# Performance work log

Measured on AMD Instinct MI355X. Metric: run time of the kernel, lower is better.

Reference implementation:

```python
import jax, jax.numpy as jnp
import numpy as np
from jax import lax

DIM = 128
N_CODEBOOKS = 8
CODEBOOK_SIZE = 2048
BATCH = 16
TOKENS = 2048


def setup_inputs() -> dict:
    key = jax.random.key(0)
    k1, k2 = jax.random.split(key)
    x = jax.random.normal(k1, (BATCH, DIM, TOKENS), dtype=jnp.float32)
    # matches nn.Parameter(torch.randn(K, D) / D**0.5) per stage, stacked
    codebooks = jax.random.normal(k2, (N_CODEBOOKS, CODEBOOK_SIZE, DIM),
                                  dtype=jnp.float32) / jnp.sqrt(jnp.float32(DIM))
    return {"x": x, "codebooks": codebooks}


def reference(x, codebooks):
    """Residual VQ forward.

    x: (B, D, T), codebooks: (n_cb, K, D)
    Returns (total_quantized (B,D,T), codes (B,n_cb,T) int32, commitment_loss scalar)
    """
    xt = jnp.transpose(x, (0, 2, 1))  # (B, T, D)

    def step(carry, cb):
        residual, total = carry  # (B,T,D) each; cb: (K,D)
        # squared euclidean distances: ||r||^2 - 2 r.c + ||c||^2 -> (B,T,K)
        dist = (jnp.sum(residual * residual, axis=-1, keepdims=True)
                - 2.0 * jnp.einsum('btd,kd->btk', residual, cb)
                + jnp.sum(cb * cb, axis=-1))
        idx = jnp.argmin(dist, axis=-1)          # (B, T)
        quantized = cb[idx]                       # gather -> (B, T, D)
        # straight-through combine
        q_st = residual + lax.stop_gradient(quantized - residual)
        total = total + q_st
        residual = residual - lax.stop_gradient(quantized)
        # F.mse_loss(residual.detach(), zeros) == mean(residual**2), detached
        loss = jnp.mean(lax.stop_gradient(residual) ** 2)
        return (residual, total), (idx.astype(jnp.int32), loss)

    init = (xt, jnp.zeros_like(xt))
    (_, total), (codes, losses) = lax.scan(step, init, codebooks)
    total_quantized = jnp.transpose(total, (0, 2, 1))   # (B, D, T)
    codes = jnp.transpose(codes, (1, 0, 2))             # (B, n_cb, T)
    commitment_loss = jnp.sum(losses)
    return total_quantized, codes, commitment_loss
```

## Files before the change

### kernel.cpp

```cpp
#include <hip/hip_runtime.h>

#define DIM 128
#define NCB 8
#define KSZ 2048
#define BATCH 16
#define TOK 2048
#define NTOK (BATCH * TOK)
#define NELEM (BATCH * DIM * TOK)
#define T_TILE 64
#define NTHR 256
#define CHUNK 64
#define NCHUNK (KSZ / CHUNK)

typedef float f32x4 __attribute__((ext_vector_type(4)));
typedef short s16x8 __attribute__((ext_vector_type(8)));

__device__ __forceinline__ unsigned short f2bf(float f) {
    unsigned u = __float_as_uint(f);
    u = (u + 0x7FFFu + ((u >> 16) & 1u)) >> 16;
    return (unsigned short)u;
}
__device__ __forceinline__ float bf2f(unsigned short h) {
    return __uint_as_float(((unsigned)h) << 16);
}

__global__ void rvq_prep_hi(const float* __restrict__ cbs,
                            unsigned short* __restrict__ ch) {
    int i = blockIdx.x * 256 + threadIdx.x;
    ch[i] = f2bf(cbs[i]);
}

__global__ void rvq_cnorm(const float* __restrict__ cbs,
                          float* __restrict__ cnorm,
                          float* __restrict__ loss_acc) {
    if (blockIdx.x == 0 && threadIdx.x == 0) *loss_acc = 0.0f;
    int k = blockIdx.x * 256 + threadIdx.x;
    const float4* row = (const float4*)(cbs + (size_t)k * DIM);
    float s = 0.0f;
#pragma unroll
    for (int i = 0; i < DIM / 4; ++i) {
        float4 v = row[i];
        s += v.x * v.x + v.y * v.y + v.z * v.z + v.w * v.w;
    }
    cnorm[k] = s;
}

__global__ __launch_bounds__(NTHR, 2) void rvq_fused(
        const float* __restrict__ x,
        const float* __restrict__ cbs,
        const unsigned short* __restrict__ ch,
        const float* __restrict__ cng,
        float* __restrict__ out,
        float* __restrict__ codes,
        float* __restrict__ loss_acc) {
    __shared__ float res_lds[T_TILE][DIM + 2];
    __shared__ unsigned short Bbuf[2][8192];
    __shared__ float mv1[T_TILE * 16];
    __shared__ float mv2[T_TILE * 16];
    __shared__ unsigned short mi1[T_TILE * 16];
    __shared__ unsigned short mi2[T_TILE * 16];

    const int tid   = threadIdx.x;
    const int lane  = tid & 63;
    const int wv    = __builtin_amdgcn_readfirstlane(tid >> 6);
    const int col16 = lane & 15;
    const int quad  = lane >> 4;

    const int token0 = blockIdx.x * T_TILE;
    const int b      = token0 >> 11;
    const int t_in_b = token0 & (TOK - 1);

    {
        const float* xb = x + (size_t)b * DIM * TOK + t_in_b;
#pragma unroll
        for (int it = 0; it < 8; ++it) {
            int idx = it * NTHR + tid;
            int d  = idx >> 4;
            int t4 = (idx & 15) * 4;
            float4 v = *(const float4*)(xb + (size_t)d * TOK + t4);
            res_lds[t4 + 0][d] = v.x;
            res_lds[t4 + 1][d] = v.y;
            res_lds[t4 + 2][d] = v.z;
            res_lds[t4 + 3][d] = v.w;
        }
    }
    __syncthreads();

    float my_loss = 0.0f;

#define STAGE_PREFETCH(cc)                                                     \
    {                                                                          \
        const unsigned short* _p = ch_s +                                      \
            ((size_t)((cc) * CHUNK + wv * 16 + col16)) * DIM + quad * 8;       \
        stg0 = *(const s16x8*)(_p + 0);                                        \
        stg1 = *(const s16x8*)(_p + 32);                                       \
        stg2 = *(const s16x8*)(_p + 64);                                       \
        stg3 = *(const s16x8*)(_p + 96);                                       \
    }

#define STAGE_WRITE(buf)                                                       \
    {                                                                          \
        *(s16x8*)&Bbuf[buf][(wv * 4 + 0) * 512 + lane * 8] = stg0;             \
        *(s16x8*)&Bbuf[buf][(wv * 4 + 1) * 512 + lane * 8] = stg1;             \
        *(s16x8*)&Bbuf[buf][(wv * 4 + 2) * 512 + lane * 8] = stg2;             \
        *(s16x8*)&Bbuf[buf][(wv * 4 + 3) * 512 + lane * 8] = stg3;             \
    }

#define COMPUTE(accv, buf)                                                     \
    {                                                                          \
        _Pragma("unroll")                                                      \
        for (int nt = 0; nt < 4; ++nt) accv[nt] = (f32x4){0.f, 0.f, 0.f, 0.f}; \
        _Pragma("unroll")                                                      \
        for (int dc = 0; dc < 4; ++dc) {                                       \
            s16x8 bh0 = *(const s16x8*)&Bbuf[buf][(0 + dc) * 512 + lane * 8];  \
            s16x8 bh1 = *(const s16x8*)&Bbuf[buf][(4 + dc) * 512 + lane * 8];  \
            s16x8 bh2 = *(const s16x8*)&Bbuf[buf][(8 + dc) * 512 + lane * 8];  \
            s16x8 bh3 = *(const s16x8*)&Bbuf[buf][(12 + dc) * 512 + lane * 8]; \
            accv[0] = __builtin_amdgcn_mfma_f32_16x16x32_bf16(ah[dc], bh0, accv[0], 0, 0, 0); \
            accv[1] = __builtin_amdgcn_mfma_f32_16x16x32_bf16(ah[dc], bh1, accv[1], 0, 0, 0); \
            accv[2] = __builtin_amdgcn_mfma_f32_16x16x32_bf16(ah[dc], bh2, accv[2], 0, 0, 0); \
            accv[3] = __builtin_amdgcn_mfma_f32_16x16x32_bf16(ah[dc], bh3, accv[3], 0, 0, 0); \
            accv[0] = __builtin_amdgcn_mfma_f32_16x16x32_bf16(al[dc], bh0, accv[0], 0, 0, 0); \
            accv[1] = __builtin_amdgcn_mfma_f32_16x16x32_bf16(al[dc], bh1, accv[1], 0, 0, 0); \
            accv[2] = __builtin_amdgcn_mfma_f32_16x16x32_bf16(al[dc], bh2, accv[2], 0, 0, 0); \
            accv[3] = __builtin_amdgcn_mfma_f32_16x16x32_bf16(al[dc], bh3, accv[3], 0, 0, 0); \
        }                                                                      \
    }

#define FOLD(accv, cc)                                                         \
    {                                                                          \
        int _ib0 = (cc) * CHUNK + col16;                                       \
        float _cn0 = cn_s[_ib0], _cn1 = cn_s[_ib0 + 16];                       \
        float _cn2 = cn_s[_ib0 + 32], _cn3 = cn_s[_ib0 + 48];                  \
        _Pragma("unroll")                                                      \
        for (int r = 0; r < 4; ++r) {                                          \
            float p0 = fmaf(-2.0f, accv[0][r], _cn0);                          \
            float p1 = fmaf(-2.0f, accv[1][r], _cn1);                          \
            float p2 = fmaf(-2.0f, accv[2][r], _cn2);                          \
            float p3 = fmaf(-2.0f, accv[3][r], _cn3);                          \
            bool c01 = p1 < p0;                                                \
            float m01 = c01 ? p1 : p0; int j01 = c01 ? _ib0 + 16 : _ib0;       \
            bool c23 = p3 < p2;                                                \
            float m23 = c23 ? p3 : p2; int j23 = c23 ? _ib0 + 48 : _ib0 + 32;  \
            bool cf = m23 < m01;                                               \
            float m = cf ? m23 : m01; int jm = cf ? j23 : j01;                 \
            bool b1 = m < v1[r];                                               \
            bool b2 = m < v2[r];                                               \
            v2[r] = b1 ? v1[r] : (b2 ? m : v2[r]);                             \
            i2[r] = b1 ? i1[r] : (b2 ? jm : i2[r]);                            \
            v1[r] = b1 ? m : v1[r];                                            \
            i1[r] = b1 ? jm : i1[r];                                           \
        }                                                                      \
    }

#pragma unroll 1
    for (int s = 0; s < NCB; ++s) {
        const unsigned short* __restrict__ ch_s = ch  + (size_t)s * KSZ * DIM;
        const float* __restrict__ cb_s = cbs + (size_t)s * KSZ * DIM;
        const float* __restrict__ cn_s = cng + (size_t)s * KSZ;

        s16x8 ah[4], al[4];
#pragma unroll
        for (int dc = 0; dc < 4; ++dc) {
            int t  = wv * 16 + col16;
            int d0 = dc * 32 + quad * 8;
            float4 u = *(const float4*)&res_lds[t][d0];
            float4 w = *(const float4*)&res_lds[t][d0 + 4];
            float e[8] = {u.x, u.y, u.z, u.w, w.x, w.y, w.z, w.w};
            s16x8 hv, lv;
#pragma unroll
            for (int j = 0; j < 8; ++j) {
                unsigned short h = f2bf(e[j]);
                hv[j] = (short)h;
                lv[j] = (short)f2bf(e[j] - bf2f(h));
            }
            ah[dc] = hv;
            al[dc] = lv;
        }

        float v1[4], v2[4]; int i1[4], i2[4];
#pragma unroll
        for (int r = 0; r < 4; ++r) {
            v1[r] = 3.4e38f; v2[r] = 3.4e38f; i1[r] = 0; i2[r] = 0;
        }

        s16x8 stg0, stg1, stg2, stg3;
        f32x4 accA[4], accB[4];

        STAGE_PREFETCH(0); STAGE_WRITE(0); __syncthreads();
        STAGE_PREFETCH(1);
        COMPUTE(accA, 0);
        STAGE_WRITE(1); __syncthreads();
#pragma unroll 1
        for (int c = 1; c < 31; c += 2) {
            STAGE_PREFETCH(c + 1);
            COMPUTE(accB, 1);
            FOLD(accA, c - 1);
            STAGE_WRITE(0);
            __syncthreads();
            STAGE_PREFETCH(c + 2);
            COMPUTE(accA, 0);
            FOLD(accB, c);
            STAGE_WRITE(1);
            __syncthreads();
        }
        COMPUTE(accB, 1);
        FOLD(accA, 30);
        FOLD(accB, 31);

#pragma unroll
        for (int r = 0; r < 4; ++r) {
            int t = wv * 16 + quad * 4 + r;
            mv1[t * 16 + col16] = v1[r];
            mi1[t * 16 + col16] = (unsigned short)i1[r];
            mv2[t * 16 + col16] = v2[r];
            mi2[t * 16 + col16] = (unsigned short)i2[r];
        }
        __syncthreads();

        const int t  = tid >> 2;
        const int cs = tid & 3;
        float bv[4] = {3.4e38f, 3.4e38f, 3.4e38f, 3.4e38f};
        int   bi[4] = {0x7FFFFFFF, 0x7FFFFFFF, 0x7FFFFFFF, 0x7FFFFFFF};
        {
            const float4 cv1 = *(const float4*)&mv1[tid * 4];
            const float4 cv2 = *(const float4*)&mv2[tid * 4];
            const unsigned short* ci1 = &mi1[tid * 4];
            const unsigned short* ci2 = &mi2[tid * 4];
            float vv[8] = {cv1.x, cv1.y, cv1.z, cv1.w,
                           cv2.x, cv2.y, cv2.z, cv2.w};
            int   ii[8] = {ci1[0], ci1[1], ci1[2], ci1[3],
                           ci2[0], ci2[1], ci2[2], ci2[3]};
#pragma unroll
            for (int c = 0; c < 8; ++c) {
                float v = vv[c]; int i = ii[c];
#pragma unroll
                for (int j = 0; j < 4; ++j) {
                    if (v < bv[j] || (v == bv[j] && i < bi[j])) {
                        float tv = bv[j]; bv[j] = v; v = tv;
                        int   ti = bi[j]; bi[j] = i; i = ti;
                    }
                }
            }
#pragma unroll
            for (int mk = 1; mk <= 2; mk <<= 1) {
                float ov[4]; int oi[4];
#pragma unroll
                for (int j = 0; j < 4; ++j) {
                    ov[j] = __shfl_xor(bv[j], mk, 64);
                    oi[j] = __shfl_xor(bi[j], mk, 64);
                }
#pragma unroll
                for (int c = 0; c < 4; ++c) {
                    float v = ov[c]; int i = oi[c];
#pragma unroll
                    for (int j = 0; j < 4; ++j) {
                        if (v < bv[j] || (v == bv[j] && i < bi[j])) {
                            float tv = bv[j]; bv[j] = v; v = tv;
                            int   ti = bi[j]; bi[j] = i; i = ti;
                        }
                    }
                }
            }
        }
        const int cand = (cs == 0) ? bi[0]
                       : (cs == 1) ? bi[1]
                       : (cs == 2) ? bi[2] : bi[3];

        {
            const float* crow = cb_s + (size_t)cand * DIM;
            float n0 = 0, n1 = 0, n2 = 0, n3 = 0;
            float a0 = 0, a1 = 0, a2 = 0, a3 = 0;
#pragma unroll 8
            for (int d4 = 0; d4 < DIM / 4; ++d4) {
                float4 r4 = *(const float4*)&res_lds[t][d4 * 4];
                float4 q4 = *(const float4*)&crow[d4 * 4];
                n0 = fmaf(r4.x, r4.x, n0); n1 = fmaf(r4.y, r4.y, n1);
                n2 = fmaf(r4.z, r4.z, n2); n3 = fmaf(r4.w, r4.w, n3);
                a0 = fmaf(r4.x, q4.x, a0); a1 = fmaf(r4.y, q4.y, a1);
                a2 = fmaf(r4.z, q4.z, a2); a3 = fmaf(r4.w, q4.w, a3);
            }
            float rn  = (n0 + n1) + (n2 + n3);
            float dot = (a0 + a1) + (a2 + a3);
            float dist = fmaf(-2.0f, dot, rn) + cn_s[cand];
            int best = cand;
#pragma unroll
            for (int mk = 1; mk <= 2; mk <<= 1) {
                float od = __shfl_xor(dist, mk, 64);
                int   oi = __shfl_xor(best, mk, 64);
                if (od < dist || (od == dist && oi < best)) {
                    dist = od; best = oi;
                }
            }
            if (cs == 0)
                codes[(size_t)b * (NCB * TOK) + (size_t)s * TOK + t_in_b + t] =
                    (float)best;
            const float* qrow = cb_s + (size_t)best * DIM;
            float lp = 0.0f;
#pragma unroll
            for (int d4 = 0; d4 < 8; ++d4) {
                int d = cs * 32 + d4 * 4;
                float4 r4 = *(const float4*)&res_lds[t][d];
                float4 q4 = *(const float4*)&qrow[d];
                float4 nr;
                nr.x = r4.x - q4.x; nr.y = r4.y - q4.y;
                nr.z = r4.z - q4.z; nr.w = r4.w - q4.w;
                *(float4*)&res_lds[t][d] = nr;
                lp += nr.x * nr.x + nr.y * nr.y + nr.z * nr.z + nr.w * nr.w;
            }
            my_loss += lp;
        }
        __syncthreads();
    }

    {
        const float* xb = x + (size_t)b * DIM * TOK + t_in_b;
        float* ob = out + (size_t)b * DIM * TOK + t_in_b;
#pragma unroll
        for (int it = 0; it < 8; ++it) {
            int idx = it * NTHR + tid;
            int d  = idx >> 4;
            int t4 = (idx & 15) * 4;
            float4 v = *(const float4*)(xb + (size_t)d * TOK + t4);
            float4 o;
            o.x = v.x - res_lds[t4 + 0][d];
            o.y = v.y - res_lds[t4 + 1][d];
            o.z = v.z - res_lds[t4 + 2][d];
            o.w = v.w - res_lds[t4 + 3][d];
            *(float4*)(ob + (size_t)d * TOK + t4) = o;
        }
    }

#pragma unroll
    for (int off = 32; off > 0; off >>= 1)
        my_loss += __shfl_down(my_loss, off, 64);
    if (lane == 0) atomicAdd(loss_acc, my_loss);
}

__global__ void rvq_loss_fin(const float* __restrict__ loss_acc,
                             float* __restrict__ loss_out) {
    *loss_out = *loss_acc * (1.0f / (float)NELEM);
}

extern "C" void kernel_launch(void* const* d_in, const int* in_sizes, int n_in,
                              void* d_out, int out_size, void* d_ws, size_t ws_size,
                              hipStream_t stream) {
    const float* x   = (const float*)d_in[0];
    const float* cbs = (const float*)d_in[1];

    float* out      = (float*)d_out;
    float* codes    = out + NELEM;
    float* loss_out = out + NELEM + (size_t)BATCH * NCB * TOK;

    float* wsf      = (float*)d_ws;
    float* loss_acc = wsf;
    unsigned short* ch = (unsigned short*)(wsf + 256);
    float* cng = (float*)(ch + (size_t)NCB * KSZ * DIM);

    hipLaunchKernelGGL(rvq_prep_hi, dim3((NCB * KSZ * DIM) / 256), dim3(256),
                       0, stream, cbs, ch);
    hipLaunchKernelGGL(rvq_cnorm, dim3((NCB * KSZ) / 256), dim3(256), 0, stream,
                       cbs, cng, loss_acc);
    hipLaunchKernelGGL(rvq_fused, dim3(NTOK / T_TILE), dim3(NTHR), 0, stream,
                       x, cbs, ch, cng, out, codes, loss_acc);
    hipLaunchKernelGGL(rvq_loss_fin, dim3(1), dim3(1), 0, stream,
                       loss_acc, loss_out);
}
```

Measured before the change: 511.5 us.

## Split codebook search across wave pairs with 512-thread blocks

Doubles the block to 512 threads. Each pair of waves shares a 16-token row group, and each wave of the pair scans one half of the codebook in 32-code chunks. The per-token top-2 merge and exact rerank are widened to 8 lanes per token, with a shared-memory handoff of the top-4 candidates. The intent is more waves in flight to hide latency. The cost is dropping the old two-accumulator software pipeline that overlapped the MFMA compute with the fold, and adding two barriers per chunk.

Result: slower. 571.8 us (+11.8%).

```diff
diff --git a/kernel.cpp b/kernel.cpp
--- a/kernel.cpp
+++ b/kernel.cpp
@@ -8,9 +8,9 @@
 #define NTOK (BATCH * TOK)
 #define NELEM (BATCH * DIM * TOK)
 #define T_TILE 64
-#define NTHR 256
-#define CHUNK 64
-#define NCHUNK (KSZ / CHUNK)
+#define NTHR 512
+#define CHUNK 32
+#define HCHUNKS 32
 
 typedef float f32x4 __attribute__((ext_vector_type(4)));
 typedef short s16x8 __attribute__((ext_vector_type(8)));
@@ -45,7 +45,7 @@
     cnorm[k] = s;
 }
 
-__global__ __launch_bounds__(NTHR, 2) void rvq_fused(
+__global__ __launch_bounds__(NTHR, 4) void rvq_fused(
         const float* __restrict__ x,
         const float* __restrict__ cbs,
         const unsigned short* __restrict__ ch,
@@ -54,17 +54,20 @@
         float* __restrict__ codes,
         float* __restrict__ loss_acc) {
     __shared__ float res_lds[T_TILE][DIM + 2];
-    __shared__ unsigned short Bbuf[2][8192];
-    __shared__ float mv1[T_TILE * 16];
-    __shared__ float mv2[T_TILE * 16];
-    __shared__ unsigned short mi1[T_TILE * 16];
-    __shared__ unsigned short mi2[T_TILE * 16];
+    __shared__ unsigned short Bbuf[2][4096];
+    __shared__ float mv1[T_TILE * 32];
+    __shared__ float mv2[T_TILE * 32];
+    __shared__ unsigned short mi1[T_TILE * 32];
+    __shared__ unsigned short mi2[T_TILE * 32];
+    __shared__ unsigned short best4s[T_TILE][4];
 
     const int tid   = threadIdx.x;
     const int lane  = tid & 63;
     const int wv    = __builtin_amdgcn_readfirstlane(tid >> 6);
     const int col16 = lane & 15;
     const int quad  = lane >> 4;
+    const int h2    = wv & 1;
+    const int wg    = wv >> 1;
 
     const int token0 = blockIdx.x * T_TILE;
     const int b      = token0 >> 11;
@@ -73,7 +76,7 @@
     {
         const float* xb = x + (size_t)b * DIM * TOK + t_in_b;
 #pragma unroll
-        for (int it = 0; it < 8; ++it) {
+        for (int it = 0; it < 4; ++it) {
             int idx = it * NTHR + tid;
             int d  = idx >> 4;
             int t4 = (idx & 15) * 4;
@@ -88,68 +91,54 @@
 
     float my_loss = 0.0f;
 
-#define STAGE_PREFETCH(cc)                                                     \
+#define STAGE_LOAD(cc)                                                         \
     {                                                                          \
-        const unsigned short* _p = ch_s +                                      \
-            ((size_t)((cc) * CHUNK + wv * 16 + col16)) * DIM + quad * 8;       \
-        stg0 = *(const s16x8*)(_p + 0);                                        \
-        stg1 = *(const s16x8*)(_p + 32);                                       \
-        stg2 = *(const s16x8*)(_p + 64);                                       \
-        stg3 = *(const s16x8*)(_p + 96);                                       \
-    }
-
-#define STAGE_WRITE(buf)                                                       \
+        const int _f0 = wg * 2, _f1 = wg * 2 + 1;                              \
+        stg0 = *(const s16x8*)(ch_s +                                          \
+            ((size_t)(h2 * 1024 + (cc) * CHUNK + (_f0 >> 2) * 16 + col16)) * DIM + \
+            ((_f0 & 3) * 32 + quad * 8));                                      \
+        stg1 = *(const s16x8*)(ch_s +                                          \
+            ((size_t)(h2 * 1024 + (cc) * CHUNK + (_f1 >> 2) * 16 + col16)) * DIM + \
+            ((_f1 & 3) * 32 + quad * 8));                                      \
+    }
+
+#define STAGE_WRITE()                                                          \
     {                                                                          \
-        *(s16x8*)&Bbuf[buf][(wv * 4 + 0) * 512 + lane * 8] = stg0;             \
-        *(s16x8*)&Bbuf[buf][(wv * 4 + 1) * 512 + lane * 8] = stg1;             \
-        *(s16x8*)&Bbuf[buf][(wv * 4 + 2) * 512 + lane * 8] = stg2;             \
-        *(s16x8*)&Bbuf[buf][(wv * 4 + 3) * 512 + lane * 8] = stg3;             \
-    }
-
-#define COMPUTE(accv, buf)                                                     \
+        *(s16x8*)&Bbuf[h2][(wg * 2 + 0) * 512 + lane * 8] = stg0;              \
+        *(s16x8*)&Bbuf[h2][(wg * 2 + 1) * 512 + lane * 8] = stg1;              \
+    }
+
+#define COMPUTE_FOLD(cc)                                                       \
     {                                                                          \
-        _Pragma("unroll")                                                      \
-        for (int nt = 0; nt < 4; ++nt) accv[nt] = (f32x4){0.f, 0.f, 0.f, 0.f}; \
+        f32x4 a0 = (f32x4){0.f, 0.f, 0.f, 0.f};                                \
+        f32x4 a1 = a0;                                                         \
         _Pragma("unroll")                                                      \
         for (int dc = 0; dc < 4; ++dc) {                                       \
-            s16x8 bh0 = *(const s16x8*)&Bbuf[buf][(0 + dc) * 512 + lane * 8];  \
-            s16x8 bh1 = *(const s16x8*)&Bbuf[buf][(4 + dc) * 512 + lane * 8];  \
-            s16x8 bh2 = *(const s16x8*)&Bbuf[buf][(8 + dc) * 512 + lane * 8];  \
-            s16x8 bh3 = *(const s16x8*)&Bbuf[buf][(12 + dc) * 512 + lane * 8]; \
-            accv[0] = __builtin_amdgcn_mfma_f32_16x16x32_bf16(ah[dc], bh0, accv[0], 0, 0, 0); \
-            accv[1] = __builtin_amdgcn_mfma_f32_16x16x32_bf16(ah[dc], bh1, accv[1], 0, 0, 0); \
-            accv[2] = __builtin_amdgcn_mfma_f32_16x16x32_bf16(ah[dc], bh2, accv[2], 0, 0, 0); \
-            accv[3] = __builtin_amdgcn_mfma_f32_16x16x32_bf16(ah[dc], bh3, accv[3], 0, 0, 0); \
-            accv[0] = __builtin_amdgcn_mfma_f32_16x16x32_bf16(al[dc], bh0, accv[0], 0, 0, 0); \
-            accv[1] = __builtin_amdgcn_mfma_f32_16x16x32_bf16(al[dc], bh1, accv[1], 0, 0, 0); \
-            accv[2] = __builtin_amdgcn_mfma_f32_16x16x32_bf16(al[dc], bh2, accv[2], 0, 0, 0); \
-            accv[3] = __builtin_amdgcn_mfma_f32_16x16x32_bf16(al[dc], bh3, accv[3], 0, 0, 0); \
+            s16x8 b0 = *(const s16x8*)&Bbuf[h2][(0 + dc) * 512 + lane * 8];    \
+            s16x8 b1 = *(const s16x8*)&Bbuf[h2][(4 + dc) * 512 + lane * 8];    \
+            a0 = __builtin_amdgcn_mfma_f32_16x16x32_bf16(ah[dc], b0, a0, 0, 0, 0); \
+            a0 = __builtin_amdgcn_mfma_f32_16x16x32_bf16(al[dc], b0, a0, 0, 0, 0); \
+            a1 = __builtin_amdgcn_mfma_f32_16x16x32_bf16(ah[dc], b1, a1, 0, 0, 0); \
+            a1 = __builtin_amdgcn_mfma_f32_16x16x32_bf16(al[dc], b1, a1, 0, 0, 0); \
         }                                                                      \
-    }
-
-#define FOLD(accv, cc)                                                         \
-    {                                                                          \
-        int _ib0 = (cc) * CHUNK + col16;                                       \
-        float _cn0 = cn_s[_ib0], _cn1 = cn_s[_ib0 + 16];                       \
-        float _cn2 = cn_s[_ib0 + 32], _cn3 = cn_s[_ib0 + 48];                  \
+        const int _ib0 = h2 * 1024 + (cc) * CHUNK + col16;                     \
+        const float _cn0 = cn_s[_ib0], _cn1 = cn_s[_ib0 + 16];                 \
         _Pragma("unroll")                                                      \
         for (int r = 0; r < 4; ++r) {                                          \
-            float p0 = fmaf(-2.0f, accv[0][r], _cn0);                          \
-            float p1 = fmaf(-2.0f, accv[1][r], _cn1);                          \
-            float p2 = fmaf(-2.0f, accv[2][r], _cn2);                          \
-            float p3 = fmaf(-2.0f, accv[3][r], _cn3);                          \
-            bool c01 = p1 < p0;                                                \
-            float m01 = c01 ? p1 : p0; int j01 = c01 ? _ib0 + 16 : _ib0;       \
-            bool c23 = p3 < p2;                                                \
-            float m23 = c23 ? p3 : p2; int j23 = c23 ? _ib0 + 48 : _ib0 + 32;  \
-            bool cf = m23 < m01;                                               \
-            float m = cf ? m23 : m01; int jm = cf ? j23 : j01;                 \
-            bool b1 = m < v1[r];                                               \
-            bool b2 = m < v2[r];                                               \
-            v2[r] = b1 ? v1[r] : (b2 ? m : v2[r]);                             \
-            i2[r] = b1 ? i1[r] : (b2 ? jm : i2[r]);                            \
-            v1[r] = b1 ? m : v1[r];                                            \
-            i1[r] = b1 ? jm : i1[r];                                           \
+            float p0 = fmaf(-2.0f, a0[r], _cn0);                               \
+            float p1 = fmaf(-2.0f, a1[r], _cn1);                               \
+            bool q1 = p0 < v1[r];                                              \
+            bool q2 = p0 < v2[r];                                              \
+            v2[r] = q1 ? v1[r] : (q2 ? p0 : v2[r]);                            \
+            i2[r] = q1 ? i1[r] : (q2 ? _ib0 : i2[r]);                          \
+            v1[r] = q1 ? p0 : v1[r];                                           \
+            i1[r] = q1 ? _ib0 : i1[r];                                         \
+            bool w1 = p1 < v1[r];                                              \
+            bool w2 = p1 < v2[r];                                              \
+            v2[r] = w1 ? v1[r] : (w2 ? p1 : v2[r]);                            \
+            i2[r] = w1 ? i1[r] : (w2 ? (_ib0 + 16) : i2[r]);                   \
+            v1[r] = w1 ? p1 : v1[r];                                           \
+            i1[r] = w1 ? (_ib0 + 16) : i1[r];                                  \
         }                                                                      \
     }
 
@@ -159,10 +148,14 @@
         const float* __restrict__ cb_s = cbs + (size_t)s * KSZ * DIM;
         const float* __restrict__ cn_s = cng + (size_t)s * KSZ;
 
+        s16x8 stg0, stg1;
+
+        STAGE_LOAD(0);
+
         s16x8 ah[4], al[4];
 #pragma unroll
         for (int dc = 0; dc < 4; ++dc) {
-            int t  = wv * 16 + col16;
+            int t  = wg * 16 + col16;
             int d0 = dc * 32 + quad * 8;
             float4 u = *(const float4*)&res_lds[t][d0];
             float4 w = *(const float4*)&res_lds[t][d0 + 4];
@@ -170,12 +163,11 @@
             s16x8 hv, lv;
 #pragma unroll
             for (int j = 0; j < 8; ++j) {
-                unsigned short h = f2bf(e[j]);
-                hv[j] = (short)h;
-                lv[j] = (short)f2bf(e[j] - bf2f(h));
-            }
-            ah[dc] = hv;
-            al[dc] = lv;
+                unsigned short hb = f2bf(e[j]);
+                hv[j] = (short)hb;
+                lv[j] = (short)f2bf(e[j] - bf2f(hb));
+            }
+            ah[dc] = hv; al[dc] = lv;
         }
 
         float v1[4], v2[4]; int i1[4], i2[4];
@@ -184,56 +176,43 @@
             v1[r] = 3.4e38f; v2[r] = 3.4e38f; i1[r] = 0; i2[r] = 0;
         }
 
-        s16x8 stg0, stg1, stg2, stg3;
-        f32x4 accA[4], accB[4];
-
-        STAGE_PREFETCH(0); STAGE_WRITE(0); __syncthreads();
-        STAGE_PREFETCH(1);
-        COMPUTE(accA, 0);
-        STAGE_WRITE(1); __syncthreads();
+        STAGE_WRITE(); __syncthreads();
 #pragma unroll 1
-        for (int c = 1; c < 31; c += 2) {
-            STAGE_PREFETCH(c + 1);
-            COMPUTE(accB, 1);
-            FOLD(accA, c - 1);
-            STAGE_WRITE(0);
+        for (int cc = 0; cc < HCHUNKS - 1; ++cc) {
+            STAGE_LOAD(cc + 1);
+            COMPUTE_FOLD(cc);
             __syncthreads();
-            STAGE_PREFETCH(c + 2);
-            COMPUTE(accA, 0);
-            FOLD(accB, c);
-            STAGE_WRITE(1);
+            STAGE_WRITE();
             __syncthreads();
         }
-        COMPUTE(accB, 1);
-        FOLD(accA, 30);
-        FOLD(accB, 31);
+        COMPUTE_FOLD(HCHUNKS - 1);
 
 #pragma unroll
         for (int r = 0; r < 4; ++r) {
-            int t = wv * 16 + quad * 4 + r;
-            mv1[t * 16 + col16] = v1[r];
-            mi1[t * 16 + col16] = (unsigned short)i1[r];
-            mv2[t * 16 + col16] = v2[r];
-            mi2[t * 16 + col16] = (unsigned short)i2[r];
+            int t = wg * 16 + quad * 4 + r;
+            int o = t * 32 + h2 * 16 + col16;
+            mv1[o] = v1[r];
+            mi1[o] = (unsigned short)i1[r];
+            mv2[o] = v2[r];
+            mi2[o] = (unsigned short)i2[r];
         }
         __syncthreads();
 
-        const int t  = tid >> 2;
-        const int cs = tid & 3;
-        float bv[4] = {3.4e38f, 3.4e38f, 3.4e38f, 3.4e38f};
-        int   bi[4] = {0x7FFFFFFF, 0x7FFFFFFF, 0x7FFFFFFF, 0x7FFFFFFF};
         {
-            const float4 cv1 = *(const float4*)&mv1[tid * 4];
-            const float4 cv2 = *(const float4*)&mv2[tid * 4];
-            const unsigned short* ci1 = &mi1[tid * 4];
-            const unsigned short* ci2 = &mi2[tid * 4];
-            float vv[8] = {cv1.x, cv1.y, cv1.z, cv1.w,
-                           cv2.x, cv2.y, cv2.z, cv2.w};
-            int   ii[8] = {ci1[0], ci1[1], ci1[2], ci1[3],
-                           ci2[0], ci2[1], ci2[2], ci2[3]};
+            const int mt = tid >> 3;
+            const int c8 = tid & 7;
+            float bv[4] = {3.4e38f, 3.4e38f, 3.4e38f, 3.4e38f};
+            int   bi[4] = {0x7FFFFFFF, 0x7FFFFFFF, 0x7FFFFFFF, 0x7FFFFFFF};
+            const float* MV = (c8 & 4) ? mv2 : mv1;
+            const unsigned short* MI = (c8 & 4) ? mi2 : mi1;
+            const int base = mt * 32 + (c8 & 3) * 8;
+            const float4 va = *(const float4*)&MV[base];
+            const float4 vb = *(const float4*)&MV[base + 4];
+            const s16x8  qi = *(const s16x8*)&MI[base];
+            float vv[8] = {va.x, va.y, va.z, va.w, vb.x, vb.y, vb.z, vb.w};
 #pragma unroll
             for (int c = 0; c < 8; ++c) {
-                float v = vv[c]; int i = ii[c];
+                float v = vv[c]; int i = (int)(unsigned short)qi[c];
 #pragma unroll
                 for (int j = 0; j < 4; ++j) {
                     if (v < bv[j] || (v == bv[j] && i < bi[j])) {
@@ -243,7 +222,7 @@
                 }
             }
 #pragma unroll
-            for (int mk = 1; mk <= 2; mk <<= 1) {
+            for (int mk = 1; mk <= 4; mk <<= 1) {
                 float ov[4]; int oi[4];
 #pragma unroll
                 for (int j = 0; j < 4; ++j) {
@@ -262,12 +241,14 @@
                     }
                 }
             }
-        }
-        const int cand = (cs == 0) ? bi[0]
-                       : (cs == 1) ? bi[1]
-                       : (cs == 2) ? bi[2] : bi[3];
+            if (c8 < 4) best4s[mt][c8] = (unsigned short)bi[c8];
+        }
+        __syncthreads();
 
         {
+            const int t  = tid >> 3;
+            const int c8 = tid & 7;
+            const int cand = best4s[t][c8 & 3];
             const float* crow = cb_s + (size_t)cand * DIM;
             float n0 = 0, n1 = 0, n2 = 0, n3 = 0;
             float a0 = 0, a1 = 0, a2 = 0, a3 = 0;
@@ -292,14 +273,14 @@
                     dist = od; best = oi;
                 }
             }
-            if (cs == 0)
+            if (c8 == 0)
                 codes[(size_t)b * (NCB * TOK) + (size_t)s * TOK + t_in_b + t] =
                     (float)best;
             const float* qrow = cb_s + (size_t)best * DIM;
             float lp = 0.0f;
 #pragma unroll
-            for (int d4 = 0; d4 < 8; ++d4) {
-                int d = cs * 32 + d4 * 4;
+            for (int k4 = 0; k4 < 4; ++k4) {
+                int d = c8 * 16 + k4 * 4;
                 float4 r4 = *(const float4*)&res_lds[t][d];
                 float4 q4 = *(const float4*)&qrow[d];
                 float4 nr;
@@ -317,7 +298,7 @@
         const float* xb = x + (size_t)b * DIM * TOK + t_in_b;
         float* ob = out + (size_t)b * DIM * TOK + t_in_b;
 #pragma unroll
-        for (int it = 0; it < 8; ++it) {
+        for (int it = 0; it < 4; ++it) {
             int idx = it * NTHR + tid;
             int d  = idx >> 4;
             int t4 = (idx & 15) * 4;
```
